# Performance work log

Hardware: AMD Instinct MI355X
Metric: run time of the kernel (lower is better)

Reference implementation:

```python
import jax, jax.numpy as jnp
import numpy as np

N_CLUSTERS = 16
D_SUB = 256          # d = n_z / n_clusters
ETA = 5.0
TEMPERATURE = 0.1
EPS = 1e-08


def _l2_normalize(x, axis):
    # matches torch F.normalize(p=2, eps=1e-8): x / max(||x||, eps)
    norm = jnp.sqrt(jnp.sum(x * x, axis=axis, keepdims=True))
    return x / jnp.maximum(norm, EPS)


def setup_inputs() -> dict:
    key = jax.random.key(0)
    k1, k2 = jax.random.split(key)
    z = jax.random.normal(k1, (16384, 4096), dtype=jnp.float32)
    D = jax.random.normal(k2, (4096, 4096), dtype=jnp.float32)
    return {"z": z, "D": D}


def reference(z, D):
    # Per-cluster loop in the original: normalize each column-slice D_i along
    # dim 0, mm, square-sum. Column-wise normalization of each slice equals
    # column-wise normalization of the whole D, so fuse into one GEMM.
    z_norm = _l2_normalize(z, axis=1)            # [N, n_z]
    D_norm = _l2_normalize(D, axis=0)            # [n_z, n_z]
    sim = z_norm @ D_norm                        # [N, n_z]
    N = sim.shape[0]
    # sum of squared similarities within each cluster's d columns
    s = jnp.sum(jnp.square(sim).reshape(N, N_CLUSTERS, D_SUB), axis=2)  # [N, K]
    s = s / TEMPERATURE + ETA * D_SUB
    s = jax.nn.softmax(s, axis=1)
    return (s, z)
```

## Files before the change

kernel.cpp:

```cpp
#include <hip/hip_runtime.h>

#define M_DIM 16384
#define N_DIM 4096
#define K_DIM 4096
#define NCLUST 16

#define BM 256
#define BN 128
#define KB4 2048
#define TKB 64
#define NT 32

typedef unsigned short u16;
typedef unsigned char u8;
typedef float floatx4 __attribute__((ext_vector_type(4)));
typedef int int4v __attribute__((ext_vector_type(4)));
typedef int int8v __attribute__((ext_vector_type(8)));

typedef const unsigned int __attribute__((address_space(1))) gu32;
typedef unsigned int __attribute__((address_space(3))) lu32;

__device__ __forceinline__ unsigned f2fp4(float x) {
  unsigned s = (__float_as_uint(x) >> 28) & 0x8u;
  float ax = fabsf(x);
  unsigned m;
  if      (ax < 0.25f) m = 0;
  else if (ax < 0.75f) m = 1;
  else if (ax < 1.25f) m = 2;
  else if (ax < 1.75f) m = 3;
  else if (ax < 2.5f)  m = 4;
  else if (ax < 3.5f)  m = 5;
  else if (ax < 5.0f)  m = 6;
  else                 m = 7;
  return s | m;
}

__global__ __launch_bounds__(256) void zero_kernel(float* __restrict__ p, int n) {
  int i = blockIdx.x * 256 + threadIdx.x;
  if (i < n) p[i] = 0.f;
}

__global__ __launch_bounds__(256) void znorm_kernel(const float* __restrict__ z,
                                                    u8* __restrict__ zn) {
  const int row = blockIdx.x;
  const int t = threadIdx.x;
  const size_t base = (size_t)row * K_DIM;
  const float4* zr = (const float4*)(z + base);
  float4 v[4];
  float ss = 0.f;
#pragma unroll
  for (int i = 0; i < 4; i++) {
    v[i] = zr[t * 4 + i];
    ss += v[i].x * v[i].x + v[i].y * v[i].y + v[i].z * v[i].z + v[i].w * v[i].w;
  }
#pragma unroll
  for (int m = 1; m <= 32; m <<= 1) ss += __shfl_xor(ss, m, 64);
  __shared__ float red[4];
  if ((t & 63) == 0) red[t >> 6] = ss;
  __syncthreads();
  float tot = red[0] + red[1] + red[2] + red[3];
  float sc = 64.0f / fmaxf(sqrtf(tot), 1e-8f);
  uint2* znr = (uint2*)(zn + (size_t)row * KB4);
  unsigned wlo = 0, whi = 0;
#pragma unroll
  for (int i = 0; i < 4; i++) {
    unsigned p = f2fp4(v[i].x * sc) | (f2fp4(v[i].y * sc) << 4) |
                 (f2fp4(v[i].z * sc) << 8) | (f2fp4(v[i].w * sc) << 12);
    if (i < 2) wlo |= p << (16 * i); else whi |= p << (16 * (i - 2));
  }
  uint2 pk; pk.x = wlo; pk.y = whi;
  znr[t] = pk;
}

__global__ __launch_bounds__(256) void colsq_kernel(const float* __restrict__ D,
                                                    float* __restrict__ colsq) {
  const int col = blockIdx.x * 256 + threadIdx.x;
  const int r0 = blockIdx.y * 128;
  float ss = 0.f;
#pragma unroll 4
  for (int r = 0; r < 128; r++) {
    float d = D[(size_t)(r0 + r) * N_DIM + col];
    ss += d * d;
  }
  atomicAdd(&colsq[col], ss);
}

__global__ __launch_bounds__(256) void dnt_kernel(const float* __restrict__ D,
                                                  const float* __restrict__ colsq,
                                                  u8* __restrict__ dnt) {
  __shared__ float tile[64][65];
  const int c0 = blockIdx.x * 64, r0 = blockIdx.y * 64;
  const int t = threadIdx.x;
  const int tr = t >> 4;
  const int tc = (t & 15) * 4;
#pragma unroll
  for (int i = 0; i < 4; i++) {
    int row = i * 16 + tr;
    float4 v = *(const float4*)(D + (size_t)(r0 + row) * N_DIM + c0 + tc);
    tile[row][tc + 0] = v.x; tile[row][tc + 1] = v.y;
    tile[row][tc + 2] = v.z; tile[row][tc + 3] = v.w;
  }
  __syncthreads();
#pragma unroll
  for (int i = 0; i < 4; i++) {
    int nl = i * 16 + tr;
    float sc = 64.0f / fmaxf(sqrtf(colsq[c0 + nl]), 1e-8f);
    u16 pk = (u16)(f2fp4(tile[tc + 0][nl] * sc) | (f2fp4(tile[tc + 1][nl] * sc) << 4) |
                   (f2fp4(tile[tc + 2][nl] * sc) << 8) | (f2fp4(tile[tc + 3][nl] * sc) << 12));
    *(u16*)(dnt + (size_t)(c0 + nl) * KB4 + ((r0 + tc) >> 1)) = pk;
  }
}

__global__ __launch_bounds__(512, 1) void gemm_kernel(const u8* __restrict__ zn,
                                                      const u8* __restrict__ dnt,
                                                      const float* __restrict__ zsrc,
                                                      float* __restrict__ out1,
                                                      float* __restrict__ s_accum) {
  __shared__ u8 ldsA[3 * BM * TKB];
  __shared__ u8 ldsB[3 * BN * TKB];

  const int t = threadIdx.x;
  const int w = t >> 6, l = t & 63;
  const int lr = l & 15, lk = l >> 4;

  const int bid = blockIdx.x;
  const int swz = (bid & 7) * 256 + (bid >> 3);
  const int bx = swz & 31, by = swz >> 5;
  const int bm = by * BM, bn = bx * BN;
  const int wm = (w >> 1) * 64, wn = (w & 1) * 64;

  const int sslot = (t & 3) ^ ((t >> 3) & 3);
  const u8* pA = zn + (size_t)(bm + (t >> 2)) * KB4 + sslot * 16;
  const u8* pB = dnt + (size_t)(bn + (t >> 2)) * KB4 + sslot * 16;

#define STAGE(OA, KT) do { \
    __builtin_amdgcn_global_load_lds((gu32*)(pA + (KT) * TKB), \
        (lu32*)&ldsA[(OA) + w * 1024], 16, 0, 0); \
    __builtin_amdgcn_global_load_lds((gu32*)(pA + (size_t)128 * KB4 + (KT) * TKB), \
        (lu32*)&ldsA[(OA) + 8192 + w * 1024], 16, 0, 0); \
    __builtin_amdgcn_global_load_lds((gu32*)(pB + (KT) * TKB), \
        (lu32*)&ldsB[((OA) >> 1) + w * 1024], 16, 0, 0); \
  } while (0)

  int aOff[4], bOff[4];
#pragma unroll
  for (int m = 0; m < 4; m++) {
    int row = wm + m * 16 + lr;
    aOff[m] = row * TKB + ((lk ^ ((row >> 1) & 3)) * 16);
  }
#pragma unroll
  for (int n = 0; n < 4; n++) {
    int row = wn + n * 16 + lr;
    bOff[n] = row * TKB + ((lk ^ ((row >> 1) & 3)) * 16);
  }

  int8v af[4], bf[4];
  floatx4 acc[4][4] = {};

#define LDFRAG(F, base, off) do { \
    int4v* _h = (int4v*)&(F); \
    _h[0] = *(const int4v*)((base) + (off)); \
    _h[1] = (int4v){0, 0, 0, 0}; \
  } while (0)

#define READ_NEXT(OA) do { \
    const u8* _ab = ldsA + (OA); \
    const u8* _bb = ldsB + ((OA) >> 1); \
    _Pragma("unroll") \
    for (int ni = 0; ni < 4; ni++) LDFRAG(bf[ni], _bb, bOff[ni]); \
    LDFRAG(af[0], _ab, aOff[0]); \
    LDFRAG(af[1], _ab, aOff[1]); \
  } while (0)

#define MFMA_H(M0) do { \
    __builtin_amdgcn_s_setprio(1); \
    _Pragma("unroll") \
    for (int mi = 0; mi < 2; mi++) \
      _Pragma("unroll") \
      for (int ni = 0; ni < 4; ni++) \
        acc[(M0) + mi][ni] = __builtin_amdgcn_mfma_scale_f32_16x16x128_f8f6f4( \
            af[(M0) + mi], bf[ni], acc[(M0) + mi][ni], 4, 4, 0, 127u, 0, 127u); \
    __builtin_amdgcn_s_setprio(0); \
  } while (0)

#define VM3 asm volatile("s_waitcnt vmcnt(3)" ::: "memory")
#define VM0 asm volatile("s_waitcnt vmcnt(0)" ::: "memory")

#define ITER(OC, STG, WT, NXT) do { \
    __builtin_amdgcn_s_barrier(); \
    __builtin_amdgcn_sched_barrier(0); \
    STG; \
    LDFRAG(af[2], ldsA + (OC), aOff[2]); \
    LDFRAG(af[3], ldsA + (OC), aOff[3]); \
    MFMA_H(0); \
    MFMA_H(2); \
    WT; \
    NXT; \
  } while (0)

#define O0 0
#define O1 16384
#define O2 32768

  STAGE(O0, 0); STAGE(O1, 1);
  VM3;
  __builtin_amdgcn_s_barrier();
  READ_NEXT(O0);

  for (int kt = 0; kt < NT - 2; kt += 3) {
    ITER(O0, STAGE(O2, kt + 2), VM3, READ_NEXT(O1));
    ITER(O1, STAGE(O0, kt + 3), VM3, READ_NEXT(O2));
    ITER(O2, STAGE(O1, kt + 4), VM3, READ_NEXT(O0));
  }
  ITER(O0, ((void)0), VM0, READ_NEXT(O1));
  ITER(O1, ((void)0), ((void)0), ((void)0));

#undef ITER
#undef O0
#undef O1
#undef O2
#undef VM3
#undef VM0
#undef MFMA_H
#undef READ_NEXT
#undef LDFRAG
#undef STAGE

  __syncthreads();
  float* red = (float*)ldsA;
#pragma unroll
  for (int m = 0; m < 4; m++) {
#pragma unroll
    for (int r = 0; r < 4; r++) {
      float v = 0.f;
#pragma unroll
      for (int n = 0; n < 4; n++) { float x = acc[m][n][r]; v += x * x; }
      v += __shfl_xor(v, 1, 64);
      v += __shfl_xor(v, 2, 64);
      v += __shfl_xor(v, 4, 64);
      v += __shfl_xor(v, 8, 64);
      if (lr == 0) {
        int lrow = wm + m * 16 + lk * 4 + r;
        red[lrow * 2 + (w & 1)] = v;
      }
    }
  }
  __syncthreads();
  if (t < 256) {
    float s = red[t * 2 + 0] + red[t * 2 + 1];
    atomicAdd(&s_accum[(size_t)(bm + t) * NCLUST + (bx >> 1)], s);
  }

  {
    const float4* cs = (const float4*)zsrc + (size_t)bid * 8192 + t;
    float4* cd = (float4*)out1 + (size_t)bid * 8192 + t;
#pragma unroll
    for (int j = 0; j < 16; j += 4) {
      float4 a0 = cs[(j + 0) * 512];
      float4 a1 = cs[(j + 1) * 512];
      float4 a2 = cs[(j + 2) * 512];
      float4 a3 = cs[(j + 3) * 512];
      cd[(j + 0) * 512] = a0;
      cd[(j + 1) * 512] = a1;
      cd[(j + 2) * 512] = a2;
      cd[(j + 3) * 512] = a3;
    }
  }
}

__global__ __launch_bounds__(256) void softmax_kernel(const float* __restrict__ s_accum,
                                                      float* __restrict__ out0) {
  int r = blockIdx.x * 256 + threadIdx.x;
  const float4* sp = (const float4*)(s_accum + (size_t)r * 16);
  float v[16];
#pragma unroll
  for (int i = 0; i < 4; i++) {
    float4 a = sp[i];
    v[i * 4 + 0] = a.x; v[i * 4 + 1] = a.y; v[i * 4 + 2] = a.z; v[i * 4 + 3] = a.w;
  }
  const float lsc = 5.9604644775390625e-7f;
  float mx = -1e30f;
#pragma unroll
  for (int i = 0; i < 16; i++) { v[i] *= lsc; mx = fmaxf(mx, v[i]); }
  float sum = 0.f;
#pragma unroll
  for (int i = 0; i < 16; i++) { v[i] = __expf(v[i] - mx); sum += v[i]; }
  float rs = 1.0f / sum;
  float4* op = (float4*)(out0 + (size_t)r * 16);
#pragma unroll
  for (int i = 0; i < 4; i++) {
    float4 a;
    a.x = v[i * 4 + 0] * rs; a.y = v[i * 4 + 1] * rs;
    a.z = v[i * 4 + 2] * rs; a.w = v[i * 4 + 3] * rs;
    op[i] = a;
  }
}

extern "C" void kernel_launch(void* const* d_in, const int* in_sizes, int n_in,
                              void* d_out, int out_size, void* d_ws, size_t ws_size,
                              hipStream_t stream) {
  const float* z = (const float*)d_in[0];
  const float* D = (const float*)d_in[1];
  float* out0 = (float*)d_out;
  float* out1 = out0 + (size_t)M_DIM * NCLUST;

  char* ws = (char*)d_ws;
  u8* zn   = (u8*)ws;
  u8* dnt  = (u8*)(ws + (size_t)M_DIM * KB4);
  float* colsq   = (float*)(ws + (size_t)M_DIM * KB4 + (size_t)N_DIM * KB4);
  float* s_accum = colsq + N_DIM;

  const int nzero = N_DIM + M_DIM * NCLUST;
  zero_kernel<<<(nzero + 255) / 256, 256, 0, stream>>>(colsq, nzero);
  znorm_kernel<<<M_DIM, 256, 0, stream>>>(z, zn);
  colsq_kernel<<<dim3(N_DIM / 256, N_DIM / 128), 256, 0, stream>>>(D, colsq);
  dnt_kernel<<<dim3(N_DIM / 64, N_DIM / 64), 256, 0, stream>>>(D, colsq, dnt);
  gemm_kernel<<<(M_DIM / BM) * (N_DIM / BN), 512, 0, stream>>>(zn, dnt, z, out1, s_accum);
  softmax_kernel<<<M_DIM / 256, 256, 0, stream>>>(s_accum, out0);
}
```

Baseline: 396.6 us.

## Interleave LDS fragment reads with MFMAs and replace atomics with partial-sum buffer

```diff
diff --git a/kernel.cpp b/kernel.cpp
--- a/kernel.cpp
+++ b/kernel.cpp
@@ -115,7 +115,7 @@
                                                       const u8* __restrict__ dnt,
                                                       const float* __restrict__ zsrc,
                                                       float* __restrict__ out1,
-                                                      float* __restrict__ s_accum) {
+                                                      float* __restrict__ s_part) {
   __shared__ u8 ldsA[3 * BM * TKB];
   __shared__ u8 ldsB[3 * BN * TKB];
 
@@ -163,13 +163,13 @@
     _h[1] = (int4v){0, 0, 0, 0}; \
   } while (0)
 
-#define READ_NEXT(OA) do { \
+#define READ_ALL(OA) do { \
     const u8* _ab = ldsA + (OA); \
     const u8* _bb = ldsB + ((OA) >> 1); \
     _Pragma("unroll") \
     for (int ni = 0; ni < 4; ni++) LDFRAG(bf[ni], _bb, bOff[ni]); \
-    LDFRAG(af[0], _ab, aOff[0]); \
-    LDFRAG(af[1], _ab, aOff[1]); \
+    _Pragma("unroll") \
+    for (int mi = 0; mi < 4; mi++) LDFRAG(af[mi], _ab, aOff[mi]); \
   } while (0)
 
 #define MFMA_H(M0) do { \
@@ -186,16 +186,24 @@
 #define VM3 asm volatile("s_waitcnt vmcnt(3)" ::: "memory")
 #define VM0 asm volatile("s_waitcnt vmcnt(0)" ::: "memory")
 
-#define ITER(OC, STG, WT, NXT) do { \
+#define ITER(OC, ON, STG, WT, RDNEXT) do { \
     __builtin_amdgcn_s_barrier(); \
     __builtin_amdgcn_sched_barrier(0); \
     STG; \
-    LDFRAG(af[2], ldsA + (OC), aOff[2]); \
-    LDFRAG(af[3], ldsA + (OC), aOff[3]); \
     MFMA_H(0); \
+    WT; \
+    if (RDNEXT) { \
+      LDFRAG(af[0], ldsA + (ON), aOff[0]); \
+      LDFRAG(af[1], ldsA + (ON), aOff[1]); \
+    } \
     MFMA_H(2); \
-    WT; \
-    NXT; \
+    if (RDNEXT) { \
+      const u8* _bb = ldsB + ((ON) >> 1); \
+      _Pragma("unroll") \
+      for (int ni = 0; ni < 4; ni++) LDFRAG(bf[ni], _bb, bOff[ni]); \
+      LDFRAG(af[2], ldsA + (ON), aOff[2]); \
+      LDFRAG(af[3], ldsA + (ON), aOff[3]); \
+    } \
   } while (0)
 
 #define O0 0
@@ -205,24 +213,24 @@
   STAGE(O0, 0); STAGE(O1, 1);
   VM3;
   __builtin_amdgcn_s_barrier();
-  READ_NEXT(O0);
+  READ_ALL(O0);
 
   for (int kt = 0; kt < NT - 2; kt += 3) {
-    ITER(O0, STAGE(O2, kt + 2), VM3, READ_NEXT(O1));
-    ITER(O1, STAGE(O0, kt + 3), VM3, READ_NEXT(O2));
-    ITER(O2, STAGE(O1, kt + 4), VM3, READ_NEXT(O0));
-  }
-  ITER(O0, ((void)0), VM0, READ_NEXT(O1));
-  ITER(O1, ((void)0), ((void)0), ((void)0));
+    ITER(O0, O1, STAGE(O2, kt + 2), VM3, 1);
+    ITER(O1, O2, STAGE(O0, kt + 3), VM3, 1);
+    ITER(O2, O0, STAGE(O1, kt + 4), VM3, 1);
+  }
+  ITER(O0, O1, ((void)0), VM0, 1);
+  ITER(O1, O1, ((void)0), ((void)0), 0);
 
 #undef ITER
+#undef READ_ALL
 #undef O0
 #undef O1
 #undef O2
 #undef VM3
 #undef VM0
 #undef MFMA_H
-#undef READ_NEXT
 #undef LDFRAG
 #undef STAGE
 
@@ -248,7 +256,7 @@
   __syncthreads();
   if (t < 256) {
     float s = red[t * 2 + 0] + red[t * 2 + 1];
-    atomicAdd(&s_accum[(size_t)(bm + t) * NCLUST + (bx >> 1)], s);
+    s_part[((size_t)(bm + t) * NCLUST + (bx >> 1)) * 2 + (bx & 1)] = s;
   }
 
   {
@@ -268,15 +276,16 @@
   }
 }
 
-__global__ __launch_bounds__(256) void softmax_kernel(const float* __restrict__ s_accum,
+__global__ __launch_bounds__(256) void softmax_kernel(const float* __restrict__ s_part,
                                                       float* __restrict__ out0) {
   int r = blockIdx.x * 256 + threadIdx.x;
-  const float4* sp = (const float4*)(s_accum + (size_t)r * 16);
+  const float4* sp = (const float4*)(s_part + (size_t)r * 32);
   float v[16];
 #pragma unroll
-  for (int i = 0; i < 4; i++) {
+  for (int i = 0; i < 8; i++) {
     float4 a = sp[i];
-    v[i * 4 + 0] = a.x; v[i * 4 + 1] = a.y; v[i * 4 + 2] = a.z; v[i * 4 + 3] = a.w;
+    v[i * 2 + 0] = a.x + a.y;
+    v[i * 2 + 1] = a.z + a.w;
   }
   const float lsc = 5.9604644775390625e-7f;
   float mx = -1e30f;
@@ -307,14 +316,13 @@
   char* ws = (char*)d_ws;
   u8* zn   = (u8*)ws;
   u8* dnt  = (u8*)(ws + (size_t)M_DIM * KB4);
-  float* colsq   = (float*)(ws + (size_t)M_DIM * KB4 + (size_t)N_DIM * KB4);
-  float* s_accum = colsq + N_DIM;
-
-  const int nzero = N_DIM + M_DIM * NCLUST;
-  zero_kernel<<<(nzero + 255) / 256, 256, 0, stream>>>(colsq, nzero);
+  float* colsq  = (float*)(ws + (size_t)M_DIM * KB4 + (size_t)N_DIM * KB4);
+  float* s_part = colsq + N_DIM;
+
+  zero_kernel<<<(N_DIM + 255) / 256, 256, 0, stream>>>(colsq, N_DIM);
   znorm_kernel<<<M_DIM, 256, 0, stream>>>(z, zn);
   colsq_kernel<<<dim3(N_DIM / 256, N_DIM / 128), 256, 0, stream>>>(D, colsq);
   dnt_kernel<<<dim3(N_DIM / 64, N_DIM / 64), 256, 0, stream>>>(D, colsq, dnt);
-  gemm_kernel<<<(M_DIM / BM) * (N_DIM / BN), 512, 0, stream>>>(zn, dnt, z, out1, s_accum);
-  softmax_kernel<<<M_DIM / 256, 256, 0, stream>>>(s_accum, out0);
-}
+  gemm_kernel<<<(M_DIM / BM) * (N_DIM / BN), 512, 0, stream>>>(zn, dnt, z, out1, s_part);
+  softmax_kernel<<<M_DIM / 256, 256, 0, stream>>>(s_part, out0);
+}
```

After: 386.3 us. 2.6% less time.
